# Kernel optimization log

Measured on AMD Instinct MI355X. Metric: run time of the kernel, lower is better.

## Reference

```python
import jax, jax.numpy as jnp
import numpy as np

NUM_HEADS = 16
HEAD_DIM = 64
HIDDEN = NUM_HEADS * HEAD_DIM


def _rope_tables(seq_len, dim, dtype):
    # inv_freq: [dim/2]; emb = cat(freqs, freqs): [S, dim]
    inv_freq = 1.0 / (10000.0 ** (jnp.arange(0, dim, 2, dtype=jnp.float32) / dim))
    t = jnp.arange(seq_len, dtype=jnp.float32)
    freqs = jnp.einsum('i,j->ij', t, inv_freq)
    emb = jnp.concatenate([freqs, freqs], axis=-1)
    return jnp.cos(emb).astype(dtype), jnp.sin(emb).astype(dtype)  # [S, dim] each


def _rotate_half(x):
    x1, x2 = jnp.split(x, 2, axis=-1)
    return jnp.concatenate([-x2, x1], axis=-1)


def setup_inputs() -> dict:
    key = jax.random.key(0)
    k1, k2, k3, k4 = jax.random.split(key, 4)
    B, S = 2, 2048
    hidden_states = jax.random.normal(k1, (B, S, HIDDEN), dtype=jnp.float32)
    scale = 0.02
    Wq = jax.random.normal(k2, (HIDDEN, HIDDEN), dtype=jnp.float32) * scale
    Wk = jax.random.normal(k3, (HIDDEN, HIDDEN), dtype=jnp.float32) * scale
    Wv = jax.random.normal(k4, (HIDDEN, HIDDEN), dtype=jnp.float32) * scale
    return {"hidden_states": hidden_states, "Wq": Wq, "Wk": Wk, "Wv": Wv}


def reference(hidden_states, Wq, Wk, Wv):
    B, S, H = hidden_states.shape
    # nn.Linear: x @ W.T ; reshape to [B, heads, S, head_dim]
    def split_heads(x):
        return x.reshape(B, S, NUM_HEADS, HEAD_DIM).transpose(0, 2, 1, 3)
    q = split_heads(hidden_states @ Wq.T)
    k = split_heads(hidden_states @ Wk.T)
    v = split_heads(hidden_states @ Wv.T)
    # inline RoPE over full head_dim
    cos, sin = _rope_tables(S, HEAD_DIM, q.dtype)  # [S, head_dim]
    cos = cos[None, None]  # [1,1,S,head_dim]
    sin = sin[None, None]
    q = q * cos + _rotate_half(q) * sin
    k = k * cos + _rotate_half(k) * sin
    # manual softmax attention
    scores = jnp.einsum('bhqd,bhkd->bhqk', q, k) / (HEAD_DIM ** 0.5)
    probs = jax.nn.softmax(scores, axis=-1)
    ctx = jnp.einsum('bhqk,bhkd->bhqd', probs, v)
    ctx = ctx.transpose(0, 2, 1, 3).reshape(B, S, H)
    return ctx
```

## Files before the change

kernel.cpp:

```cpp
#include <hip/hip_runtime.h>
#include <math.h>

#define NHEADS 16
#define HDIM   64
#define HID    1024
#define BATCH  2
#define SEQ    2048
#define NX (BATCH*SEQ*HID)
#define NW (HID*HID)

typedef unsigned short u16;
typedef __attribute__((ext_vector_type(8))) short  bf16x8;
typedef __attribute__((ext_vector_type(8))) unsigned short u16x8;
typedef __attribute__((ext_vector_type(4))) float  f32x4;


__device__ __forceinline__ void split8(const float* xf, bf16x8& hi, bf16x8& lo) {
#pragma unroll
    for (int j = 0; j < 8; j++) {
        unsigned u = __float_as_uint(xf[j]);
        hi[j] = (short)(u >> 16);
        float hf = __uint_as_float(u & 0xFFFF0000u);
        lo[j] = (short)(__float_as_uint(xf[j] - hf) >> 16);
    }
}
__device__ __forceinline__ void split1(float v, u16& h, u16& l) {
    unsigned u = __float_as_uint(v);
    h = (u16)(u >> 16);
    l = (u16)(__float_as_uint(v - __uint_as_float(u & 0xFFFF0000u)) >> 16);
}

__global__ void rope_tables_kernel(float* __restrict__ ct, float* __restrict__ st) {
    int idx = blockIdx.x * 256 + threadIdx.x;
    if (idx >= SEQ * HDIM) return;
    int s  = idx >> 6;
    int dh = idx & 63;
    int i  = dh & 31;
    float inv = exp2f(-(float)i * (13.28771237954945f / 32.0f));
    float fr  = (float)s * inv;
    ct[idx] = cosf(fr);
    st[idx] = sinf(fr);
}

__global__ void split_kernel(const float* __restrict__ X,
                             const float* __restrict__ W0,
                             const float* __restrict__ W1,
                             const float* __restrict__ W2,
                             u16* __restrict__ Xhi, u16* __restrict__ Xlo,
                             u16* __restrict__ Whi, u16* __restrict__ Wlo)
{
    long idx = ((long)blockIdx.x * 256 + threadIdx.x) * 4;
    if (idx >= (long)NX + 3L * NW) return;
    const float* src; u16* dh; u16* dl; long off;
    if (idx < NX) { src = X; dh = Xhi; dl = Xlo; off = idx; }
    else {
        long rr = idx - NX;
        int wi = (int)(rr >> 20);
        off = rr & (NW - 1);
        src = (wi == 0) ? W0 : ((wi == 1) ? W1 : W2);
        dh = Whi + (size_t)wi * NW;
        dl = Wlo + (size_t)wi * NW;
    }
    const int r = (int)(off >> 10);
    const int k = (int)(off & 1023);
    const size_t fo = ((size_t)(r >> 4) * 32 + (k >> 5)) * 512
                    + (size_t)((k >> 3) & 3) * 128 + (size_t)(r & 15) * 8 + (k & 7);
    float4 v = *(const float4*)(src + off);
    const float* vf = (const float*)&v;
    ushort4 h4, l4;
    u16* hp = (u16*)&h4; u16* lp = (u16*)&l4;
#pragma unroll
    for (int e = 0; e < 4; e++) split1(vf[e], hp[e], lp[e]);
    *(ushort4*)(dh + fo) = h4;
    *(ushort4*)(dl + fo) = l4;
}

__global__ __launch_bounds__(256, 2) void qkv_mfma_kernel(
    const u16* __restrict__ Xhi, const u16* __restrict__ Xlo,
    const u16* __restrict__ Whi, const u16* __restrict__ Wlo,
    const float* __restrict__ ct, const float* __restrict__ st,
    u16* __restrict__ Qhi, u16* __restrict__ Qlo,
    u16* __restrict__ Khi, u16* __restrict__ Klo,
    u16* __restrict__ Vhi, u16* __restrict__ Vlo)
{
    __shared__ unsigned vtr[64][129];

    const int t    = threadIdx.x;
    const int lane = t & 63;
    const int w    = t >> 6;
    const int lx   = lane & 15;
    const int quad = lane >> 4;
    const int proj = blockIdx.z;
    const int n0   = blockIdx.x * 128;
    const int m0   = blockIdx.y * 128;

    const u16* __restrict__ Wph = Whi + (size_t)proj * NW;
    const u16* __restrict__ Wpl = Wlo + (size_t)proj * NW;

    const int am = (w & 1) * 64;
    const int bn = (w >> 1) * 64;
    const int lp = quad * 128 + lx * 8;

    const u16 *pAh[4], *pAl[4], *pBh[4], *pBl[4];
#pragma unroll
    for (int i = 0; i < 4; i++) {
        const size_t o = ((size_t)(((m0 + am) >> 4) + i) * 32) * 512 + lp;
        pAh[i] = Xhi + o; pAl[i] = Xlo + o;
    }
#pragma unroll
    for (int j = 0; j < 4; j++) {
        const size_t o = ((size_t)(((n0 + bn) >> 4) + j) * 32) * 512 + lp;
        pBh[j] = Wph + o; pBl[j] = Wpl + o;
    }

    f32x4 acc[4][4];
#pragma unroll
    for (int i = 0; i < 4; i++)
#pragma unroll
        for (int j = 0; j < 4; j++) acc[i][j] = (f32x4){0.f, 0.f, 0.f, 0.f};

    bf16x8 cah[4], cal[4], cbh[4], cbl[4];
#pragma unroll
    for (int i = 0; i < 4; i++) { cah[i] = *(const bf16x8*)(pAh[i]); cal[i] = *(const bf16x8*)(pAl[i]); }
#pragma unroll
    for (int j = 0; j < 4; j++) { cbh[j] = *(const bf16x8*)(pBh[j]); cbl[j] = *(const bf16x8*)(pBl[j]); }

#pragma unroll 1
    for (int kt = 0; kt < HID; kt += 32) {
        const int ko = (kt + 32 < HID) ? ((kt + 32) >> 5) * 512 : 0;
        bf16x8 nah[4], nal[4], nbh[4], nbl[4];
#pragma unroll
        for (int i = 0; i < 4; i++) { nah[i] = *(const bf16x8*)(pAh[i] + ko); nal[i] = *(const bf16x8*)(pAl[i] + ko); }
#pragma unroll
        for (int j = 0; j < 4; j++) { nbh[j] = *(const bf16x8*)(pBh[j] + ko); nbl[j] = *(const bf16x8*)(pBl[j] + ko); }

#pragma unroll
        for (int j = 0; j < 4; j++)
#pragma unroll
            for (int i = 0; i < 4; i++) {
                acc[i][j] = __builtin_amdgcn_mfma_f32_16x16x32_bf16(cah[i], cbh[j], acc[i][j], 0, 0, 0);
                acc[i][j] = __builtin_amdgcn_mfma_f32_16x16x32_bf16(cal[i], cbh[j], acc[i][j], 0, 0, 0);
                acc[i][j] = __builtin_amdgcn_mfma_f32_16x16x32_bf16(cah[i], cbl[j], acc[i][j], 0, 0, 0);
            }
#pragma unroll
        for (int i = 0; i < 4; i++) { cah[i] = nah[i]; cal[i] = nal[i]; }
#pragma unroll
        for (int j = 0; j < 4; j++) { cbh[j] = nbh[j]; cbl[j] = nbl[j]; }
    }

    const int b      = m0 >> 11;
    const int head   = (n0 >> 6) + (w >> 1);
    const int m_base = m0 + am;

    if (proj < 2) {
#pragma unroll
        for (int i = 0; i < 4; i++) {
#pragma unroll
            for (int r = 0; r < 4; r++) {
                const int s = (m_base + i * 16 + quad * 4 + r) & 2047;
                const float* ctr = ct + s * HDIM;
                const float* str = st + s * HDIM;
                float nv[4];
#pragma unroll
                for (int j = 0; j < 4; j++) {
                    const int dh = j * 16 + lx;
                    const float c  = ctr[dh];
                    const float sn = str[dh];
                    const float x  = acc[i][j][r];
                    const float p  = acc[i][j ^ 2][r];
                    nv[j] = (j < 2) ? (x * c - p * sn) : (x * c + p * sn);
                }
#pragma unroll
                for (int j = 0; j < 4; j++) acc[i][j][r] = nv[j];
            }
        }
        u16* dh_ = (proj == 0) ? Qhi : Khi;
        u16* dl_ = (proj == 0) ? Qlo : Klo;
        const size_t obase = (size_t)(b * NHEADS + head) * SEQ * HDIM;
#pragma unroll
        for (int i = 0; i < 4; i++)
#pragma unroll
            for (int r = 0; r < 4; r++) {
                const int s   = (m_base + i * 16 + quad * 4 + r) & 2047;
                const int rb  = s >> 4;
                const int lxq = s & 15;
#pragma unroll
                for (int j = 0; j < 4; j++) {
                    const size_t fo = obase + ((size_t)rb * 2 + (j >> 1)) * 512
                                    + (size_t)((j & 1) * 2 + (lx >> 3)) * 128
                                    + (size_t)lxq * 8 + (lx & 7);
                    u16 hh, ll;
                    split1(acc[i][j][r], hh, ll);
                    dh_[fo] = hh;
                    dl_[fo] = ll;
                }
            }
    } else {
#pragma unroll 1
        for (int pass = 0; pass < 2; pass++) {
            __syncthreads();
            if ((w & 1) == pass) {
#pragma unroll
                for (int i = 0; i < 4; i++)
#pragma unroll
                    for (int j = 0; j < 4; j++)
#pragma unroll
                        for (int r = 0; r < 4; r++) {
                            const int ml = i * 16 + quad * 4 + r;
                            const int nl = bn + j * 16 + lx;
                            const float v = acc[i][j][r];
                            unsigned u  = __float_as_uint(v);
                            unsigned hi = u & 0xFFFF0000u;
                            unsigned lo = __float_as_uint(v - __uint_as_float(hi)) >> 16;
                            vtr[ml][nl] = hi | lo;
                        }
            }
            __syncthreads();
            {
                const int d      = t >> 1;
                const int sh     = (t & 1) * 32;
                const int headv  = (n0 >> 6) + (d >> 6);
                const int dd     = d & 63;
                const size_t vbase = (size_t)(b * NHEADS + headv) * SEQ * HDIM;
                const int s0base = (m0 & 2047) + pass * 64 + sh;
#pragma unroll
                for (int k = 0; k < 4; k++) {
                    const int s0 = s0base + k * 8;
                    u16x8 hv, lv;
#pragma unroll
                    for (int e = 0; e < 8; e++) {
                        unsigned u = vtr[sh + k * 8 + e][d];
                        hv[e] = (u16)(u >> 16);
                        lv[e] = (u16)(u & 0xFFFFu);
                    }
                    const size_t fo = vbase + ((size_t)(dd >> 4) * 64 + (s0 >> 5)) * 512
                                    + (size_t)((s0 >> 3) & 3) * 128 + (size_t)(dd & 15) * 8;
                    *(u16x8*)(Vhi + fo) = hv;
                    *(u16x8*)(Vlo + fo) = lv;
                }
            }
        }
    }
}

__global__ __launch_bounds__(256, 2) void attn_kernel(
    const u16* __restrict__ Qhi, const u16* __restrict__ Qlo,
    const u16* __restrict__ Khi, const u16* __restrict__ Klo,
    const u16* __restrict__ Vhi, const u16* __restrict__ Vlo,
    float* __restrict__ OUT)
{
    __shared__ float PS[4][32][68];

    const int t    = threadIdx.x;
    const int lane = t & 63;
    const int w    = t >> 6;
    const int lx   = lane & 15;
    const int quad = lane >> 4;

    const int q0 = blockIdx.x * 128;
    const int h  = blockIdx.y;
    const int b  = blockIdx.z;
    const size_t base = (size_t)(b * NHEADS + h) * SEQ * HDIM;
    const int lp = quad * 128 + lx * 8;

    bf16x8 qh[2][2], ql[2][2];
#pragma unroll
    for (int a = 0; a < 2; a++)
#pragma unroll
        for (int ks = 0; ks < 2; ks++) {
            const size_t fo = base + ((size_t)((q0 >> 4) + w * 2 + a) * 2 + ks) * 512 + lp;
            qh[a][ks] = *(const bf16x8*)(Qhi + fo);
            ql[a][ks] = *(const bf16x8*)(Qlo + fo);
        }

    f32x4 O[2][4];
    float l_part[2][4];
#pragma unroll
    for (int a = 0; a < 2; a++) {
#pragma unroll
        for (int dt = 0; dt < 4; dt++) O[a][dt] = (f32x4){0.f,0.f,0.f,0.f};
#pragma unroll
        for (int r = 0; r < 4; r++) l_part[a][r] = 0.f;
    }

#pragma unroll 1
    for (int kt = 0; kt < SEQ; kt += 64) {
        bf16x8 kh[2][4], kl[2][4];
#pragma unroll
        for (int c = 0; c < 4; c++)
#pragma unroll
            for (int ks = 0; ks < 2; ks++) {
                const size_t fo = base + ((size_t)((kt >> 4) + c) * 2 + ks) * 512 + lp;
                kh[ks][c] = *(const bf16x8*)(Khi + fo);
                kl[ks][c] = *(const bf16x8*)(Klo + fo);
            }

#pragma unroll
        for (int a = 0; a < 2; a++) {
#pragma unroll
            for (int c = 0; c < 4; c++) {
                f32x4 acc = (f32x4){0.f,0.f,0.f,0.f};
#pragma unroll
                for (int ks = 0; ks < 2; ks++) {
                    acc = __builtin_amdgcn_mfma_f32_16x16x32_bf16(qh[a][ks], kh[ks][c], acc, 0, 0, 0);
                    acc = __builtin_amdgcn_mfma_f32_16x16x32_bf16(ql[a][ks], kh[ks][c], acc, 0, 0, 0);
                    acc = __builtin_amdgcn_mfma_f32_16x16x32_bf16(qh[a][ks], kl[ks][c], acc, 0, 0, 0);
                }
#pragma unroll
                for (int r = 0; r < 4; r++) {
                    float p = exp2f(acc[r] * 0.18033688011112042f);
                    l_part[a][r] += p;
                    PS[w][a * 16 + quad * 4 + r][c * 16 + lx] = p;
                }
            }
        }

        bf16x8 vh[2][4], vl[2][4];
#pragma unroll
        for (int dt = 0; dt < 4; dt++)
#pragma unroll
            for (int ks2 = 0; ks2 < 2; ks2++) {
                const size_t fo = base + ((size_t)dt * 64 + (kt >> 5) + ks2) * 512 + lp;
                vh[ks2][dt] = *(const bf16x8*)(Vhi + fo);
                vl[ks2][dt] = *(const bf16x8*)(Vlo + fo);
            }

#pragma unroll
        for (int a = 0; a < 2; a++) {
#pragma unroll
            for (int ks2 = 0; ks2 < 2; ks2++) {
                const float* ps = &PS[w][a * 16 + lx][ks2 * 32 + quad * 8];
                float pf[8];
                *(float4*)&pf[0] = *(const float4*)ps;
                *(float4*)&pf[4] = *(const float4*)(ps + 4);
                bf16x8 phi, plo;
                split8(pf, phi, plo);
#pragma unroll
                for (int dt = 0; dt < 4; dt++) {
                    O[a][dt] = __builtin_amdgcn_mfma_f32_16x16x32_bf16(phi, vh[ks2][dt], O[a][dt], 0, 0, 0);
                    O[a][dt] = __builtin_amdgcn_mfma_f32_16x16x32_bf16(plo, vh[ks2][dt], O[a][dt], 0, 0, 0);
                    O[a][dt] = __builtin_amdgcn_mfma_f32_16x16x32_bf16(phi, vl[ks2][dt], O[a][dt], 0, 0, 0);
                }
            }
        }
    }

    float linv[2][4];
#pragma unroll
    for (int a = 0; a < 2; a++)
#pragma unroll
        for (int r = 0; r < 4; r++) {
            float l = l_part[a][r];
            l += __shfl_xor(l, 1);
            l += __shfl_xor(l, 2);
            l += __shfl_xor(l, 4);
            l += __shfl_xor(l, 8);
            linv[a][r] = 1.f / l;
        }

    float* Po = &PS[0][0][0];
    __syncthreads();
#pragma unroll
    for (int a = 0; a < 2; a++)
#pragma unroll
        for (int dt = 0; dt < 4; dt++)
#pragma unroll
            for (int r = 0; r < 4; r++)
                Po[(size_t)(w * 32 + a * 16 + quad * 4 + r) * 68 + dt * 16 + lx] =
                    O[a][dt][r] * linv[a][r];
    __syncthreads();
    {
        const int q    = t >> 1;
        const int half = t & 1;
        const float* prow = Po + (size_t)q * 68 + half * 32;
        float* dst = OUT + ((size_t)(b * SEQ + q0 + q)) * HID + h * HDIM + half * 32;
#pragma unroll
        for (int e = 0; e < 8; e++)
            ((float4*)dst)[e] = ((const float4*)prow)[e];
    }
}

extern "C" void kernel_launch(void* const* d_in, const int* in_sizes, int n_in,
                              void* d_out, int out_size, void* d_ws, size_t ws_size,
                              hipStream_t stream)
{
    const float* X  = (const float*)d_in[0];
    const float* Wq = (const float*)d_in[1];
    const float* Wk = (const float*)d_in[2];
    const float* Wv = (const float*)d_in[3];
    float* out = (float*)d_out;

    const size_t qkv_elems = (size_t)BATCH * NHEADS * SEQ * HDIM;
    char* wsb = (char*)d_ws;
    float* ct  = (float*)wsb;
    float* st  = ct + (size_t)SEQ * HDIM;
    u16* Xhi = (u16*)(st + (size_t)SEQ * HDIM);
    u16* Xlo = Xhi + (size_t)NX;
    u16* Whi = Xlo + (size_t)NX;
    u16* Wlo = Whi + 3 * (size_t)NW;
    u16* Qhi = Wlo + 3 * (size_t)NW;
    u16* Qlo = Qhi + qkv_elems;
    u16* Khi = Qlo + qkv_elems;
    u16* Klo = Khi + qkv_elems;
    u16* Vhi = Klo + qkv_elems;
    u16* Vlo = Vhi + qkv_elems;

    rope_tables_kernel<<<(SEQ * HDIM + 255) / 256, 256, 0, stream>>>(ct, st);

    const long tot = (long)NX + 3L * NW;
    split_kernel<<<(int)((tot / 4 + 255) / 256), 256, 0, stream>>>(
        X, Wq, Wk, Wv, Xhi, Xlo, Whi, Wlo);

    qkv_mfma_kernel<<<dim3(HID / 128, (BATCH * SEQ) / 128, 3), 256, 0, stream>>>(
        Xhi, Xlo, Whi, Wlo, ct, st, Qhi, Qlo, Khi, Klo, Vhi, Vlo);

    attn_kernel<<<dim3(SEQ / 128, NHEADS, BATCH), 256, 0, stream>>>(
        Qhi, Qlo, Khi, Klo, Vhi, Vlo, out);
}
```

Baseline: 335.2 us.

## Halve attention query tile per block and fold softmax scale into Q

The attention kernel now gives each block 64 query rows instead of 128, so each wave handles one 16-row tile. That halves the register and LDS footprint and raises the launch-bounds occupancy hint from 2 to 4 blocks per CU, with twice as many blocks launched. The softmax scale (1/sqrt(d) times log2 e) is multiplied into Q in the projection epilogue, which drops a multiply per score in the inner loop. In exchange, each block reloads the full K and V streams for half as many queries, doubling global/L2 traffic for K and V, and scaling Q before the hi/lo bf16 split slightly changes rounding.

```diff
diff --git a/kernel.cpp b/kernel.cpp
--- a/kernel.cpp
+++ b/kernel.cpp
@@ -176,6 +176,7 @@
         }
         u16* dh_ = (proj == 0) ? Qhi : Khi;
         u16* dl_ = (proj == 0) ? Qlo : Klo;
+        const float qscale = (proj == 0) ? 0.18033688011112042f : 1.0f;
         const size_t obase = (size_t)(b * NHEADS + head) * SEQ * HDIM;
 #pragma unroll
         for (int i = 0; i < 4; i++)
@@ -190,7 +191,7 @@
                                     + (size_t)((j & 1) * 2 + (lx >> 3)) * 128
                                     + (size_t)lxq * 8 + (lx & 7);
                     u16 hh, ll;
-                    split1(acc[i][j][r], hh, ll);
+                    split1(acc[i][j][r] * qscale, hh, ll);
                     dh_[fo] = hh;
                     dl_[fo] = ll;
                 }
@@ -243,13 +244,13 @@
     }
 }
 
-__global__ __launch_bounds__(256, 2) void attn_kernel(
+__global__ __launch_bounds__(256, 4) void attn_kernel(
     const u16* __restrict__ Qhi, const u16* __restrict__ Qlo,
     const u16* __restrict__ Khi, const u16* __restrict__ Klo,
     const u16* __restrict__ Vhi, const u16* __restrict__ Vlo,
     float* __restrict__ OUT)
 {
-    __shared__ float PS[4][32][68];
+    __shared__ float PS[4][16][68];
 
     const int t    = threadIdx.x;
     const int lane = t & 63;
@@ -257,31 +258,26 @@
     const int lx   = lane & 15;
     const int quad = lane >> 4;
 
-    const int q0 = blockIdx.x * 128;
+    const int q0 = blockIdx.x * 64;
     const int h  = blockIdx.y;
     const int b  = blockIdx.z;
     const size_t base = (size_t)(b * NHEADS + h) * SEQ * HDIM;
     const int lp = quad * 128 + lx * 8;
 
-    bf16x8 qh[2][2], ql[2][2];
-#pragma unroll
-    for (int a = 0; a < 2; a++)
-#pragma unroll
-        for (int ks = 0; ks < 2; ks++) {
-            const size_t fo = base + ((size_t)((q0 >> 4) + w * 2 + a) * 2 + ks) * 512 + lp;
-            qh[a][ks] = *(const bf16x8*)(Qhi + fo);
-            ql[a][ks] = *(const bf16x8*)(Qlo + fo);
-        }
-
-    f32x4 O[2][4];
-    float l_part[2][4];
-#pragma unroll
-    for (int a = 0; a < 2; a++) {
-#pragma unroll
-        for (int dt = 0; dt < 4; dt++) O[a][dt] = (f32x4){0.f,0.f,0.f,0.f};
-#pragma unroll
-        for (int r = 0; r < 4; r++) l_part[a][r] = 0.f;
-    }
+    bf16x8 qh[2], ql[2];
+#pragma unroll
+    for (int ks = 0; ks < 2; ks++) {
+        const size_t fo = base + ((size_t)((q0 >> 4) + w) * 2 + ks) * 512 + lp;
+        qh[ks] = *(const bf16x8*)(Qhi + fo);
+        ql[ks] = *(const bf16x8*)(Qlo + fo);
+    }
+
+    f32x4 O[4];
+    float l_part[4];
+#pragma unroll
+    for (int dt = 0; dt < 4; dt++) O[dt] = (f32x4){0.f,0.f,0.f,0.f};
+#pragma unroll
+    for (int r = 0; r < 4; r++) l_part[r] = 0.f;
 
 #pragma unroll 1
     for (int kt = 0; kt < SEQ; kt += 64) {
@@ -296,22 +292,19 @@
             }
 
 #pragma unroll
-        for (int a = 0; a < 2; a++) {
-#pragma unroll
-            for (int c = 0; c < 4; c++) {
-                f32x4 acc = (f32x4){0.f,0.f,0.f,0.f};
-#pragma unroll
-                for (int ks = 0; ks < 2; ks++) {
-                    acc = __builtin_amdgcn_mfma_f32_16x16x32_bf16(qh[a][ks], kh[ks][c], acc, 0, 0, 0);
-                    acc = __builtin_amdgcn_mfma_f32_16x16x32_bf16(ql[a][ks], kh[ks][c], acc, 0, 0, 0);
-                    acc = __builtin_amdgcn_mfma_f32_16x16x32_bf16(qh[a][ks], kl[ks][c], acc, 0, 0, 0);
-                }
-#pragma unroll
-                for (int r = 0; r < 4; r++) {
-                    float p = exp2f(acc[r] * 0.18033688011112042f);
-                    l_part[a][r] += p;
-                    PS[w][a * 16 + quad * 4 + r][c * 16 + lx] = p;
-                }
+        for (int c = 0; c < 4; c++) {
+            f32x4 acc = (f32x4){0.f,0.f,0.f,0.f};
+#pragma unroll
+            for (int ks = 0; ks < 2; ks++) {
+                acc = __builtin_amdgcn_mfma_f32_16x16x32_bf16(qh[ks], kh[ks][c], acc, 0, 0, 0);
+                acc = __builtin_amdgcn_mfma_f32_16x16x32_bf16(ql[ks], kh[ks][c], acc, 0, 0, 0);
+                acc = __builtin_amdgcn_mfma_f32_16x16x32_bf16(qh[ks], kl[ks][c], acc, 0, 0, 0);
+            }
+#pragma unroll
+            for (int r = 0; r < 4; r++) {
+                float p = exp2f(acc[r]);
+                l_part[r] += p;
+                PS[w][quad * 4 + r][c * 16 + lx] = p;
             }
         }
 
@@ -326,56 +319,48 @@
             }
 
 #pragma unroll
-        for (int a = 0; a < 2; a++) {
-#pragma unroll
-            for (int ks2 = 0; ks2 < 2; ks2++) {
-                const float* ps = &PS[w][a * 16 + lx][ks2 * 32 + quad * 8];
-                float pf[8];
-                *(float4*)&pf[0] = *(const float4*)ps;
-                *(float4*)&pf[4] = *(const float4*)(ps + 4);
-                bf16x8 phi, plo;
-                split8(pf, phi, plo);
-#pragma unroll
-                for (int dt = 0; dt < 4; dt++) {
-                    O[a][dt] = __builtin_amdgcn_mfma_f32_16x16x32_bf16(phi, vh[ks2][dt], O[a][dt], 0, 0, 0);
-                    O[a][dt] = __builtin_amdgcn_mfma_f32_16x16x32_bf16(plo, vh[ks2][dt], O[a][dt], 0, 0, 0);
-                    O[a][dt] = __builtin_amdgcn_mfma_f32_16x16x32_bf16(phi, vl[ks2][dt], O[a][dt], 0, 0, 0);
-                }
+        for (int ks2 = 0; ks2 < 2; ks2++) {
+            const float* ps = &PS[w][lx][ks2 * 32 + quad * 8];
+            float pf[8];
+            *(float4*)&pf[0] = *(const float4*)ps;
+            *(float4*)&pf[4] = *(const float4*)(ps + 4);
+            bf16x8 phi, plo;
+            split8(pf, phi, plo);
+#pragma unroll
+            for (int dt = 0; dt < 4; dt++) {
+                O[dt] = __builtin_amdgcn_mfma_f32_16x16x32_bf16(phi, vh[ks2][dt], O[dt], 0, 0, 0);
+                O[dt] = __builtin_amdgcn_mfma_f32_16x16x32_bf16(plo, vh[ks2][dt], O[dt], 0, 0, 0);
+                O[dt] = __builtin_amdgcn_mfma_f32_16x16x32_bf16(phi, vl[ks2][dt], O[dt], 0, 0, 0);
             }
         }
     }
 
-    float linv[2][4];
-#pragma unroll
-    for (int a = 0; a < 2; a++)
-#pragma unroll
-        for (int r = 0; r < 4; r++) {
-            float l = l_part[a][r];
-            l += __shfl_xor(l, 1);
-            l += __shfl_xor(l, 2);
-            l += __shfl_xor(l, 4);
-            l += __shfl_xor(l, 8);
-            linv[a][r] = 1.f / l;
-        }
+    float linv[4];
+#pragma unroll
+    for (int r = 0; r < 4; r++) {
+        float l = l_part[r];
+        l += __shfl_xor(l, 1);
+        l += __shfl_xor(l, 2);
+        l += __shfl_xor(l, 4);
+        l += __shfl_xor(l, 8);
+        linv[r] = 1.f / l;
+    }
 
     float* Po = &PS[0][0][0];
-    __syncthreads();
-#pragma unroll
-    for (int a = 0; a < 2; a++)
-#pragma unroll
-        for (int dt = 0; dt < 4; dt++)
-#pragma unroll
-            for (int r = 0; r < 4; r++)
-                Po[(size_t)(w * 32 + a * 16 + quad * 4 + r) * 68 + dt * 16 + lx] =
-                    O[a][dt][r] * linv[a][r];
+#pragma unroll
+    for (int dt = 0; dt < 4; dt++)
+#pragma unroll
+        for (int r = 0; r < 4; r++)
+            Po[(size_t)(w * 16 + quad * 4 + r) * 68 + dt * 16 + lx] =
+                O[dt][r] * linv[r];
     __syncthreads();
     {
-        const int q    = t >> 1;
-        const int half = t & 1;
-        const float* prow = Po + (size_t)q * 68 + half * 32;
-        float* dst = OUT + ((size_t)(b * SEQ + q0 + q)) * HID + h * HDIM + half * 32;
-#pragma unroll
-        for (int e = 0; e < 8; e++)
+        const int q    = t >> 2;
+        const int part = t & 3;
+        const float* prow = Po + (size_t)q * 68 + part * 16;
+        float* dst = OUT + ((size_t)(b * SEQ + q0 + q)) * HID + h * HDIM + part * 16;
+#pragma unroll
+        for (int e = 0; e < 4; e++)
             ((float4*)dst)[e] = ((const float4*)prow)[e];
     }
 }
@@ -414,6 +399,6 @@
     qkv_mfma_kernel<<<dim3(HID / 128, (BATCH * SEQ) / 128, 3), 256, 0, stream>>>(
         Xhi, Xlo, Whi, Wlo, ct, st, Qhi, Qlo, Khi, Klo, Vhi, Vlo);
 
-    attn_kernel<<<dim3(SEQ / 128, NHEADS, BATCH), 256, 0, stream>>>(
+    attn_kernel<<<dim3(SEQ / 64, NHEADS, BATCH), 256, 0, stream>>>(
         Qhi, Qlo, Khi, Klo, Vhi, Vlo, out);
 }
```

Result: slower. 503.2 us (+50.1%).

## Double-buffer K tiles in attention loop and fold softmax scale into Q

Applied to the files above, without the earlier changes.

The attention inner loop now prefetches the next K tile into a second register buffer while the current tile's QK^T and PV work runs, using a two-step unrolled loop with ping-pong buffers. V loads are moved ahead of the QK MFMAs so their latency is hidden as well. The softmax scale (1/sqrt(d) * log2 e) is folded into Q at projection time, which removes a multiply per score. The extra K buffer raises register pressure and could lower occupancy. Scaling Q before the hi/lo bf16 split slightly changes rounding.

```diff
diff --git a/kernel.cpp b/kernel.cpp
--- a/kernel.cpp
+++ b/kernel.cpp
@@ -176,6 +176,7 @@
         }
         u16* dh_ = (proj == 0) ? Qhi : Khi;
         u16* dl_ = (proj == 0) ? Qlo : Klo;
+        const float qscale = (proj == 0) ? 0.18033688011112042f : 1.0f;
         const size_t obase = (size_t)(b * NHEADS + head) * SEQ * HDIM;
 #pragma unroll
         for (int i = 0; i < 4; i++)
@@ -190,7 +191,7 @@
                                     + (size_t)((j & 1) * 2 + (lx >> 3)) * 128
                                     + (size_t)lxq * 8 + (lx & 7);
                     u16 hh, ll;
-                    split1(acc[i][j][r], hh, ll);
+                    split1(acc[i][j][r] * qscale, hh, ll);
                     dh_[fo] = hh;
                     dl_[fo] = ll;
                 }
@@ -283,38 +284,19 @@
         for (int r = 0; r < 4; r++) l_part[a][r] = 0.f;
     }
 
-#pragma unroll 1
-    for (int kt = 0; kt < SEQ; kt += 64) {
-        bf16x8 kh[2][4], kl[2][4];
-#pragma unroll
-        for (int c = 0; c < 4; c++)
-#pragma unroll
-            for (int ks = 0; ks < 2; ks++) {
-                const size_t fo = base + ((size_t)((kt >> 4) + c) * 2 + ks) * 512 + lp;
-                kh[ks][c] = *(const bf16x8*)(Khi + fo);
-                kl[ks][c] = *(const bf16x8*)(Klo + fo);
-            }
-
-#pragma unroll
-        for (int a = 0; a < 2; a++) {
-#pragma unroll
-            for (int c = 0; c < 4; c++) {
-                f32x4 acc = (f32x4){0.f,0.f,0.f,0.f};
-#pragma unroll
-                for (int ks = 0; ks < 2; ks++) {
-                    acc = __builtin_amdgcn_mfma_f32_16x16x32_bf16(qh[a][ks], kh[ks][c], acc, 0, 0, 0);
-                    acc = __builtin_amdgcn_mfma_f32_16x16x32_bf16(ql[a][ks], kh[ks][c], acc, 0, 0, 0);
-                    acc = __builtin_amdgcn_mfma_f32_16x16x32_bf16(qh[a][ks], kl[ks][c], acc, 0, 0, 0);
-                }
-#pragma unroll
-                for (int r = 0; r < 4; r++) {
-                    float p = exp2f(acc[r] * 0.18033688011112042f);
-                    l_part[a][r] += p;
-                    PS[w][a * 16 + quad * 4 + r][c * 16 + lx] = p;
-                }
-            }
-        }
-
+    bf16x8 kAh[2][4], kAl[2][4], kBh[2][4], kBl[2][4];
+#pragma unroll
+    for (int c = 0; c < 4; c++)
+#pragma unroll
+        for (int ks = 0; ks < 2; ks++) {
+            const size_t fo = base + ((size_t)c * 2 + ks) * 512 + lp;
+            kAh[ks][c] = *(const bf16x8*)(Khi + fo);
+            kAl[ks][c] = *(const bf16x8*)(Klo + fo);
+        }
+
+    auto tile_body = [&](bf16x8 (&ckh)[2][4], bf16x8 (&ckl)[2][4],
+                         bf16x8 (&nkh)[2][4], bf16x8 (&nkl)[2][4],
+                         int kt, int ktn) {
         bf16x8 vh[2][4], vl[2][4];
 #pragma unroll
         for (int dt = 0; dt < 4; dt++)
@@ -323,6 +305,35 @@
                 const size_t fo = base + ((size_t)dt * 64 + (kt >> 5) + ks2) * 512 + lp;
                 vh[ks2][dt] = *(const bf16x8*)(Vhi + fo);
                 vl[ks2][dt] = *(const bf16x8*)(Vlo + fo);
+            }
+
+#pragma unroll
+        for (int a = 0; a < 2; a++) {
+#pragma unroll
+            for (int c = 0; c < 4; c++) {
+                f32x4 acc = (f32x4){0.f,0.f,0.f,0.f};
+#pragma unroll
+                for (int ks = 0; ks < 2; ks++) {
+                    acc = __builtin_amdgcn_mfma_f32_16x16x32_bf16(qh[a][ks], ckh[ks][c], acc, 0, 0, 0);
+                    acc = __builtin_amdgcn_mfma_f32_16x16x32_bf16(ql[a][ks], ckh[ks][c], acc, 0, 0, 0);
+                    acc = __builtin_amdgcn_mfma_f32_16x16x32_bf16(qh[a][ks], ckl[ks][c], acc, 0, 0, 0);
+                }
+#pragma unroll
+                for (int r = 0; r < 4; r++) {
+                    float p = exp2f(acc[r]);
+                    l_part[a][r] += p;
+                    PS[w][a * 16 + quad * 4 + r][c * 16 + lx] = p;
+                }
+            }
+        }
+
+#pragma unroll
+        for (int c = 0; c < 4; c++)
+#pragma unroll
+            for (int ks = 0; ks < 2; ks++) {
+                const size_t fo = base + ((size_t)((ktn >> 4) + c) * 2 + ks) * 512 + lp;
+                nkh[ks][c] = *(const bf16x8*)(Khi + fo);
+                nkl[ks][c] = *(const bf16x8*)(Klo + fo);
             }
 
 #pragma unroll
@@ -343,6 +354,12 @@
                 }
             }
         }
+    };
+
+#pragma unroll 1
+    for (int kt = 0; kt < SEQ; kt += 128) {
+        tile_body(kAh, kAl, kBh, kBl, kt,       kt + 64);
+        tile_body(kBh, kBl, kAh, kAl, kt + 64, (kt + 128) & (SEQ - 1));
     }
 
     float linv[2][4];
```

New measurement: 309.6 us. 7.6% less time.
